# Kernel optimization log

Measured on AMD Instinct MI355X. Metric: run time of the kernel, lower is better.

Reference implementation:

```python
import jax, jax.numpy as jnp
import numpy as np

D = 1024
H = 16
DH = D // H  # 64

def setup_inputs() -> dict:
    key = jax.random.key(0)
    ks = jax.random.split(key, 9)
    B, S = 2, 2048
    s = 1.0 / np.sqrt(D)
    return {
        "embed": jax.random.normal(ks[0], (B, S, D), dtype=jnp.float32),
        "Wq": jax.random.normal(ks[1], (D, D), dtype=jnp.float32) * s,
        "Wk": jax.random.normal(ks[2], (D, D), dtype=jnp.float32) * s,
        "Wv": jax.random.normal(ks[3], (D, D), dtype=jnp.float32) * s,
        "bv": jax.random.normal(ks[4], (D,), dtype=jnp.float32) * 0.01,
        "W1": jax.random.normal(ks[5], (2 * D, D), dtype=jnp.float32) * s,
        "b1": jax.random.normal(ks[6], (2 * D,), dtype=jnp.float32) * 0.01,
        "W2": jax.random.normal(ks[7], (D, 2 * D), dtype=jnp.float32) * (1.0 / np.sqrt(2 * D)),
        "b2": jax.random.normal(ks[8], (D,), dtype=jnp.float32) * 0.01,
    }

def reference(embed, Wq, Wk, Wv, bv, W1, b1, W2, b2):
    B, S, _ = embed.shape
    # torch nn.Linear: y = x @ W.T (+ b)
    Q = embed @ Wq.T                      # [B,S,D]
    K = embed @ Wk.T                      # [B,S,D]
    V = embed @ Wv.T + bv                 # [B,S,D]
    # split heads: the per-head python loop in the original is a vmap over H
    Qh = Q.reshape(B, S, H, DH)
    Kh = K.reshape(B, S, H, DH)
    Vh = V.reshape(B, S, H, DH)
    scores = jnp.einsum('bqhd,bkhd->bhqk', Qh, Kh) / np.sqrt(DH)
    attn = jax.nn.softmax(scores, axis=-1)          # [B,H,S,S]
    out = jnp.einsum('bhqk,bkhd->bqhd', attn, Vh).reshape(B, S, D)
    # FFN (use_ffn)
    out = jax.nn.relu(out @ W1.T + b1) @ W2.T + b2
    # residual (use_residue)
    return out + embed
```

## Files before the change

### kernel.cpp

```cpp
#include <hip/hip_runtime.h>
#include <hip/hip_bf16.h>

typedef unsigned short u16;
typedef unsigned int u32;
typedef __attribute__((ext_vector_type(8))) short short8;
typedef __attribute__((ext_vector_type(4))) short short4v;
typedef __attribute__((ext_vector_type(4))) float f32x4;
typedef __attribute__((ext_vector_type(4))) u16 u16x4;
typedef __attribute__((ext_vector_type(4))) u32 u32x4;

__device__ __forceinline__ u16 f2bf(float f) {
  unsigned u = __builtin_bit_cast(unsigned, f);
  u = (u + 0x7FFFu + ((u >> 16) & 1u)) >> 16;
  return (u16)u;
}

__device__ __forceinline__ u32 cvt_pk_bf16(float lo, float hi) {
  u32 r;
  asm("v_cvt_pk_bf16_f32 %0, %1, %2" : "=v"(r) : "v"(lo), "v"(hi));
  return r;
}

__device__ __forceinline__ void gload16(const void* g, void* l) {
  __builtin_amdgcn_global_load_lds(
      (const __attribute__((address_space(1))) void*)g,
      (__attribute__((address_space(3))) void*)l, 16, 0, 0);
}

__global__ __launch_bounds__(256) void cvt_all(
    const float* __restrict__ e, const float* __restrict__ wq,
    const float* __restrict__ wk, const float* __restrict__ wv,
    const float* __restrict__ w1, const float* __restrict__ w2,
    u16* __restrict__ ebf, u16* __restrict__ wqkv,
    u16* __restrict__ w1b, u16* __restrict__ w2b)
{
  int i = blockIdx.x * 256 + threadIdx.x;
  const float* src;
  u16* dst;
  if (i < 1048576)       { src = e;  dst = ebf; }
  else if (i < 1310720)  { src = wq; dst = wqkv;           i -= 1048576; }
  else if (i < 1572864)  { src = wk; dst = wqkv + 1048576; i -= 1310720; }
  else if (i < 1835008)  { src = wv; dst = wqkv + 2097152; i -= 1572864; }
  else if (i < 2359296)  { src = w1; dst = w1b;            i -= 1835008; }
  else                   { src = w2; dst = w2b;            i -= 2359296; }
  const float4 v = reinterpret_cast<const float4*>(src)[i];
  u16x4 o = { f2bf(v.x), f2bf(v.y), f2bf(v.z), f2bf(v.w) };
  *reinterpret_cast<u16x4*>(dst + (size_t)i * 4) = o;
}

template<int MODE, int BM>
__global__ __launch_bounds__(256, 3) void gemm_bt(
    const u16* __restrict__ A, const u16* __restrict__ W,
    const float* __restrict__ bias, const float* __restrict__ resid,
    void* __restrict__ out0, void* __restrict__ out1, void* __restrict__ out2,
    int M, int N, int K)
{
  constexpr int II = BM / 32;
  __shared__ __align__(16) u16 At[BM * 64];
  __shared__ __align__(16) u16 Bt[128 * 64];
  const int tid = threadIdx.x, lane = tid & 63, wid = tid >> 6;
  const int g = lane >> 4, c = lane & 15;
  const int wr = (wid >> 1) * (BM / 2), wc = (wid & 1) * 64;
  const int m0 = blockIdx.y * BM, n0 = blockIdx.x * 128;
  const int lrow = lane >> 3;
  const int lch = (lane & 7) ^ lrow;
  const int rsw = c & 7;

  f32x4 acc[II][4];
  #pragma unroll
  for (int i = 0; i < II; i++)
    #pragma unroll
    for (int j = 0; j < 4; j++)
      acc[i][j] = (f32x4){0.f, 0.f, 0.f, 0.f};

  const u16* Ab = A + (size_t)m0 * K;
  const u16* Wb = W + (size_t)n0 * K;

  for (int k0 = 0; k0 < K; k0 += 64) {
    __syncthreads();
    #pragma unroll
    for (int i = 0; i < II; i++) {
      const int r0 = (wid * II + i) * 8;
      gload16(Ab + (size_t)(r0 + lrow) * K + k0 + lch * 8, &At[r0 * 64]);
    }
    #pragma unroll
    for (int i = 0; i < 4; i++) {
      const int r0 = (wid * 4 + i) * 8;
      gload16(Wb + (size_t)(r0 + lrow) * K + k0 + lch * 8, &Bt[r0 * 64]);
    }
    __syncthreads();
    #pragma unroll
    for (int kh = 0; kh < 2; kh++) {
      short8 af[II], bw[4];
      #pragma unroll
      for (int i = 0; i < II; i++)
        af[i] = *reinterpret_cast<const short8*>(
            &At[(wr + i * 16 + c) * 64 + (((g + 4 * kh) ^ rsw) * 8)]);
      #pragma unroll
      for (int j = 0; j < 4; j++)
        bw[j] = *reinterpret_cast<const short8*>(
            &Bt[(wc + j * 16 + c) * 64 + (((g + 4 * kh) ^ rsw) * 8)]);
      #pragma unroll
      for (int i = 0; i < II; i++)
        #pragma unroll
        for (int j = 0; j < 4; j++)
          acc[i][j] = __builtin_amdgcn_mfma_f32_16x16x32_bf16(af[i], bw[j], acc[i][j], 0, 0, 0);
    }
  }

  #pragma unroll
  for (int i = 0; i < II; i++) {
    #pragma unroll
    for (int j = 0; j < 4; j++) {
      const int n = n0 + wc + j * 16 + c;
      const int mb = m0 + wr + i * 16 + g * 4;
      if (MODE == 1) {
        const int seg = n >> 10, nn = n & 1023;
        const int h = nn >> 6, d = nn & 63;
        const int bb = mb >> 11, s = mb & 2047;
        if (seg == 2) {
          const float bval = bias[nn];
          u16x4 o;
          #pragma unroll
          for (int r = 0; r < 4; r++) o[r] = f2bf(acc[i][j][r] + bval);
          *reinterpret_cast<u16x4*>(reinterpret_cast<u16*>(out2) +
              ((size_t)((bb << 4) + h) * 64 + d) * 2048 + s) = o;
        } else {
          u16* dst = reinterpret_cast<u16*>(seg ? out1 : out0);
          const float sc = seg ? 1.0f : 0.18033688f;
          #pragma unroll
          for (int r = 0; r < 4; r++)
            dst[((size_t)((bb << 4) + h) * 2048 + s + r) * 64 + d] = f2bf(acc[i][j][r] * sc);
        }
      } else if (MODE == 3) {
        const float bval = bias[n];
        #pragma unroll
        for (int r = 0; r < 4; r++) {
          float v = fmaxf(acc[i][j][r] + bval, 0.f);
          reinterpret_cast<u16*>(out0)[(size_t)(mb + r) * N + n] = f2bf(v);
        }
      } else {
        const float bval = bias[n];
        #pragma unroll
        for (int r = 0; r < 4; r++) {
          const int m = mb + r;
          reinterpret_cast<float*>(out0)[(size_t)m * N + n] =
              acc[i][j][r] + bval + resid[(size_t)m * N + n];
        }
      }
    }
  }
}

__global__ __launch_bounds__(256, 4) void attn_kernel(
    const u16* __restrict__ Qh, const u16* __restrict__ Kh,
    const u16* __restrict__ Vt, u16* __restrict__ ao)
{
  __shared__ __align__(16) u16 Kt[2][64 * 64];
  __shared__ __align__(16) u16 Vl[2][64 * 64];

  const int tid = threadIdx.x;
  const int lane = tid & 63, wid = tid >> 6;
  const int g = lane >> 4, c = lane & 15;
  const int bh = blockIdx.y;
  const int q0 = blockIdx.x * 64 + wid * 16;
  const int lrow = lane >> 3;
  const int lch = (lane & 7) ^ lrow;
  const int rsw = c & 7;

  const u16* qrow = Qh + ((size_t)bh * 2048 + q0 + c) * 64;
  const short8 bqa = *reinterpret_cast<const short8*>(qrow + g * 8);
  const short8 bqb = *reinterpret_cast<const short8*>(qrow + 32 + g * 8);

  f32x4 acc[4];
  #pragma unroll
  for (int dt = 0; dt < 4; dt++) acc[dt] = (f32x4){0.f, 0.f, 0.f, 0.f};
  float l_run = 0.f;

  const u16* Kb = Kh + (size_t)bh * 2048 * 64;
  const u16* Vb = Vt + (size_t)bh * 64 * 2048;

  auto stage = [&](int buf, int t0) {
    #pragma unroll
    for (int i = 0; i < 2; i++) {
      const int r0 = (wid * 2 + i) * 8;
      gload16(Kb + (size_t)(t0 + r0 + lrow) * 64 + lch * 8, &Kt[buf][r0 * 64]);
    }
    #pragma unroll
    for (int i = 0; i < 2; i++) {
      const int r0 = (wid * 2 + i) * 8;
      gload16(Vb + (size_t)(r0 + lrow) * 2048 + t0 + lch * 8, &Vl[buf][r0 * 64]);
    }
  };

  stage(0, 0);

  int cur = 0;
  for (int t0 = 0; t0 < 2048; t0 += 64, cur ^= 1) {
    __syncthreads();
    if (t0 + 64 < 2048) stage(cur ^ 1, t0 + 64);

    #pragma unroll
    for (int cp = 0; cp < 2; cp++) {
      f32x4 sv[2];
      __builtin_amdgcn_s_setprio(1);
      #pragma unroll
      for (int h = 0; h < 2; h++) {
        const u16* kr = &Kt[cur][(cp * 32 + h * 16 + c) * 64];
        short8 ka  = *reinterpret_cast<const short8*>(kr + ((g ^ rsw) * 8));
        short8 ka2 = *reinterpret_cast<const short8*>(kr + (((g + 4) ^ rsw) * 8));
        f32x4 z = (f32x4){0.f, 0.f, 0.f, 0.f};
        z = __builtin_amdgcn_mfma_f32_16x16x32_bf16(ka, bqa, z, 0, 0, 0);
        z = __builtin_amdgcn_mfma_f32_16x16x32_bf16(ka2, bqb, z, 0, 0, 0);
        sv[h] = z;
      }
      __builtin_amdgcn_s_setprio(0);

      float p[8];
      #pragma unroll
      for (int i = 0; i < 8; i++)
        p[i] = __builtin_amdgcn_exp2f(sv[i >> 2][i & 3]);
      l_run += ((p[0] + p[1]) + (p[2] + p[3])) + ((p[4] + p[5]) + (p[6] + p[7]));
      u32x4 w;
      #pragma unroll
      for (int k = 0; k < 4; k++)
        w[k] = cvt_pk_bf16(p[2 * k], p[2 * k + 1]);
      const short8 pk = __builtin_bit_cast(short8, w);

      __builtin_amdgcn_s_setprio(1);
      #pragma unroll
      for (int dt = 0; dt < 4; dt++) {
        const u16* vr = &Vl[cur][(dt * 16 + c) * 64];
        const int ch0 = cp * 4 + (g >> 1);
        const int sub = (g & 1) * 4;
        short4v va  = *reinterpret_cast<const short4v*>(vr + ((ch0 ^ rsw) * 8) + sub);
        short4v vb2 = *reinterpret_cast<const short4v*>(vr + (((ch0 + 2) ^ rsw) * 8) + sub);
        short8 vf = __builtin_shufflevector(va, vb2, 0, 1, 2, 3, 4, 5, 6, 7);
        acc[dt] = __builtin_amdgcn_mfma_f32_16x16x32_bf16(pk, vf, acc[dt], 0, 0, 0);
      }
      __builtin_amdgcn_s_setprio(0);
    }
  }

  float l = l_run;
  l += __shfl_xor(l, 16);
  l += __shfl_xor(l, 32);
  float lq[4];
  #pragma unroll
  for (int r = 0; r < 4; r++) lq[r] = 1.0f / __shfl(l, g * 4 + r);
  u16* ob = ao + (size_t)(bh >> 4) * 2048 * 1024 + (bh & 15) * 64;
  #pragma unroll
  for (int dt = 0; dt < 4; dt++)
    #pragma unroll
    for (int r = 0; r < 4; r++) {
      const size_t q = q0 + g * 4 + r;
      ob[q * 1024 + dt * 16 + c] = f2bf(acc[dt][r] * lq[r]);
    }
}

extern "C" void kernel_launch(void* const* d_in, const int* in_sizes, int n_in,
                              void* d_out, int out_size, void* d_ws, size_t ws_size,
                              hipStream_t stream) {
  const float* embed = (const float*)d_in[0];
  const float* Wq = (const float*)d_in[1];
  const float* Wk = (const float*)d_in[2];
  const float* Wv = (const float*)d_in[3];
  const float* bv = (const float*)d_in[4];
  const float* W1 = (const float*)d_in[5];
  const float* b1 = (const float*)d_in[6];
  const float* W2 = (const float*)d_in[7];
  const float* b2 = (const float*)d_in[8];

  char* ws = (char*)d_ws;
  u16* ebf  = (u16*)ws;  ws += (size_t)4096 * 1024 * 2;
  u16* wqkv = (u16*)ws;  ws += (size_t)3072 * 1024 * 2;
  u16* w1b  = (u16*)ws;  ws += (size_t)2048 * 1024 * 2;
  u16* w2b  = (u16*)ws;  ws += (size_t)1024 * 2048 * 2;
  u16* Qh   = (u16*)ws;  ws += (size_t)4096 * 1024 * 2;
  u16* Kh   = (u16*)ws;  ws += (size_t)4096 * 1024 * 2;
  u16* Vt   = (u16*)ws;  ws += (size_t)4096 * 1024 * 2;
  u16* ao   = (u16*)ws;  ws += (size_t)4096 * 1024 * 2;
  u16* h1   = (u16*)ws;  ws += (size_t)4096 * 2048 * 2;

  dim3 blk(256);
  cvt_all<<<dim3(11264), blk, 0, stream>>>(embed, Wq, Wk, Wv, W1, W2,
                                           ebf, wqkv, w1b, w2b);
  gemm_bt<1, 128><<<dim3(24, 32), blk, 0, stream>>>(
      ebf, wqkv, bv, nullptr, Qh, Kh, Vt, 4096, 3072, 1024);
  attn_kernel<<<dim3(32, 32), blk, 0, stream>>>(Qh, Kh, Vt, ao);
  gemm_bt<3, 128><<<dim3(16, 32), blk, 0, stream>>>(
      ao, w1b, b1, nullptr, h1, nullptr, nullptr, 4096, 2048, 1024);
  gemm_bt<4, 64><<<dim3(8, 64), blk, 0, stream>>>(
      h1, w2b, b2, embed, d_out, nullptr, nullptr, 4096, 1024, 2048);
}
```

Baseline: 154.5 us.

## Process two query tiles per wave in attention and permute V layout

Measured after the change: 144.3 us. 1.07x faster.

```diff
diff --git a/kernel.cpp b/kernel.cpp
--- a/kernel.cpp
+++ b/kernel.cpp
@@ -4,7 +4,6 @@
 typedef unsigned short u16;
 typedef unsigned int u32;
 typedef __attribute__((ext_vector_type(8))) short short8;
-typedef __attribute__((ext_vector_type(4))) short short4v;
 typedef __attribute__((ext_vector_type(4))) float f32x4;
 typedef __attribute__((ext_vector_type(4))) u16 u16x4;
 typedef __attribute__((ext_vector_type(4))) u32 u32x4;
@@ -123,8 +122,10 @@
           u16x4 o;
           #pragma unroll
           for (int r = 0; r < 4; r++) o[r] = f2bf(acc[i][j][r] + bval);
+          const int s32 = s & 31;
+          const int t2 = (s & ~31) + ((s32 >> 2) & 3) * 8 + ((s32 >> 4) & 1) * 4;
           *reinterpret_cast<u16x4*>(reinterpret_cast<u16*>(out2) +
-              ((size_t)((bb << 4) + h) * 64 + d) * 2048 + s) = o;
+              ((size_t)((bb << 4) + h) * 64 + d) * 2048 + t2) = o;
         } else {
           u16* dst = reinterpret_cast<u16*>(seg ? out1 : out0);
           const float sc = seg ? 1.0f : 0.18033688f;
@@ -152,7 +153,7 @@
   }
 }
 
-__global__ __launch_bounds__(256, 4) void attn_kernel(
+__global__ __launch_bounds__(256, 2) void attn_kernel(
     const u16* __restrict__ Qh, const u16* __restrict__ Kh,
     const u16* __restrict__ Vt, u16* __restrict__ ao)
 {
@@ -163,19 +164,27 @@
   const int lane = tid & 63, wid = tid >> 6;
   const int g = lane >> 4, c = lane & 15;
   const int bh = blockIdx.y;
-  const int q0 = blockIdx.x * 64 + wid * 16;
+  const int q0 = blockIdx.x * 128 + wid * 32;
   const int lrow = lane >> 3;
   const int lch = (lane & 7) ^ lrow;
   const int rsw = c & 7;
 
-  const u16* qrow = Qh + ((size_t)bh * 2048 + q0 + c) * 64;
-  const short8 bqa = *reinterpret_cast<const short8*>(qrow + g * 8);
-  const short8 bqb = *reinterpret_cast<const short8*>(qrow + 32 + g * 8);
-
-  f32x4 acc[4];
-  #pragma unroll
-  for (int dt = 0; dt < 4; dt++) acc[dt] = (f32x4){0.f, 0.f, 0.f, 0.f};
-  float l_run = 0.f;
+  short8 bq[2][2];
+  #pragma unroll
+  for (int qt = 0; qt < 2; qt++) {
+    const u16* qrow = Qh + ((size_t)bh * 2048 + q0 + qt * 16 + c) * 64;
+    bq[qt][0] = *reinterpret_cast<const short8*>(qrow + g * 8);
+    bq[qt][1] = *reinterpret_cast<const short8*>(qrow + 32 + g * 8);
+  }
+
+  f32x4 acc[2][4];
+  #pragma unroll
+  for (int qt = 0; qt < 2; qt++)
+    #pragma unroll
+    for (int dt = 0; dt < 4; dt++)
+      acc[qt][dt] = (f32x4){0.f, 0.f, 0.f, 0.f};
+  f32x4 accl[2] = {(f32x4){0.f, 0.f, 0.f, 0.f}, (f32x4){0.f, 0.f, 0.f, 0.f}};
+  const short8 ones = {0x3F80, 0x3F80, 0x3F80, 0x3F80, 0x3F80, 0x3F80, 0x3F80, 0x3F80};
 
   const u16* Kb = Kh + (size_t)bh * 2048 * 64;
   const u16* Vb = Vt + (size_t)bh * 64 * 2048;
@@ -202,60 +211,65 @@
 
     #pragma unroll
     for (int cp = 0; cp < 2; cp++) {
-      f32x4 sv[2];
+      f32x4 sv[2][2];
       __builtin_amdgcn_s_setprio(1);
       #pragma unroll
       for (int h = 0; h < 2; h++) {
         const u16* kr = &Kt[cur][(cp * 32 + h * 16 + c) * 64];
         short8 ka  = *reinterpret_cast<const short8*>(kr + ((g ^ rsw) * 8));
         short8 ka2 = *reinterpret_cast<const short8*>(kr + (((g + 4) ^ rsw) * 8));
-        f32x4 z = (f32x4){0.f, 0.f, 0.f, 0.f};
-        z = __builtin_amdgcn_mfma_f32_16x16x32_bf16(ka, bqa, z, 0, 0, 0);
-        z = __builtin_amdgcn_mfma_f32_16x16x32_bf16(ka2, bqb, z, 0, 0, 0);
-        sv[h] = z;
+        #pragma unroll
+        for (int qt = 0; qt < 2; qt++) {
+          f32x4 z = (f32x4){0.f, 0.f, 0.f, 0.f};
+          z = __builtin_amdgcn_mfma_f32_16x16x32_bf16(ka, bq[qt][0], z, 0, 0, 0);
+          z = __builtin_amdgcn_mfma_f32_16x16x32_bf16(ka2, bq[qt][1], z, 0, 0, 0);
+          sv[qt][h] = z;
+        }
       }
       __builtin_amdgcn_s_setprio(0);
 
-      float p[8];
-      #pragma unroll
-      for (int i = 0; i < 8; i++)
-        p[i] = __builtin_amdgcn_exp2f(sv[i >> 2][i & 3]);
-      l_run += ((p[0] + p[1]) + (p[2] + p[3])) + ((p[4] + p[5]) + (p[6] + p[7]));
-      u32x4 w;
-      #pragma unroll
-      for (int k = 0; k < 4; k++)
-        w[k] = cvt_pk_bf16(p[2 * k], p[2 * k + 1]);
-      const short8 pk = __builtin_bit_cast(short8, w);
+      short8 pk[2];
+      #pragma unroll
+      for (int qt = 0; qt < 2; qt++) {
+        float p[8];
+        #pragma unroll
+        for (int i = 0; i < 8; i++)
+          p[i] = __builtin_amdgcn_exp2f(sv[qt][i >> 2][i & 3]);
+        u32x4 w;
+        #pragma unroll
+        for (int k = 0; k < 4; k++)
+          w[k] = cvt_pk_bf16(p[2 * k], p[2 * k + 1]);
+        pk[qt] = __builtin_bit_cast(short8, w);
+      }
 
       __builtin_amdgcn_s_setprio(1);
       #pragma unroll
       for (int dt = 0; dt < 4; dt++) {
-        const u16* vr = &Vl[cur][(dt * 16 + c) * 64];
-        const int ch0 = cp * 4 + (g >> 1);
-        const int sub = (g & 1) * 4;
-        short4v va  = *reinterpret_cast<const short4v*>(vr + ((ch0 ^ rsw) * 8) + sub);
-        short4v vb2 = *reinterpret_cast<const short4v*>(vr + (((ch0 + 2) ^ rsw) * 8) + sub);
-        short8 vf = __builtin_shufflevector(va, vb2, 0, 1, 2, 3, 4, 5, 6, 7);
-        acc[dt] = __builtin_amdgcn_mfma_f32_16x16x32_bf16(pk, vf, acc[dt], 0, 0, 0);
-      }
+        const short8 vf = *reinterpret_cast<const short8*>(
+            &Vl[cur][(dt * 16 + c) * 64 + (((cp * 4 + g) ^ rsw) * 8)]);
+        acc[0][dt] = __builtin_amdgcn_mfma_f32_16x16x32_bf16(pk[0], vf, acc[0][dt], 0, 0, 0);
+        acc[1][dt] = __builtin_amdgcn_mfma_f32_16x16x32_bf16(pk[1], vf, acc[1][dt], 0, 0, 0);
+      }
+      accl[0] = __builtin_amdgcn_mfma_f32_16x16x32_bf16(pk[0], ones, accl[0], 0, 0, 0);
+      accl[1] = __builtin_amdgcn_mfma_f32_16x16x32_bf16(pk[1], ones, accl[1], 0, 0, 0);
       __builtin_amdgcn_s_setprio(0);
     }
   }
 
-  float l = l_run;
-  l += __shfl_xor(l, 16);
-  l += __shfl_xor(l, 32);
-  float lq[4];
-  #pragma unroll
-  for (int r = 0; r < 4; r++) lq[r] = 1.0f / __shfl(l, g * 4 + r);
   u16* ob = ao + (size_t)(bh >> 4) * 2048 * 1024 + (bh & 15) * 64;
   #pragma unroll
-  for (int dt = 0; dt < 4; dt++)
-    #pragma unroll
-    for (int r = 0; r < 4; r++) {
-      const size_t q = q0 + g * 4 + r;
-      ob[q * 1024 + dt * 16 + c] = f2bf(acc[dt][r] * lq[r]);
-    }
+  for (int qt = 0; qt < 2; qt++) {
+    float lq[4];
+    #pragma unroll
+    for (int r = 0; r < 4; r++) lq[r] = 1.0f / accl[qt][r];
+    #pragma unroll
+    for (int dt = 0; dt < 4; dt++)
+      #pragma unroll
+      for (int r = 0; r < 4; r++) {
+        const size_t q = q0 + qt * 16 + g * 4 + r;
+        ob[q * 1024 + dt * 16 + c] = f2bf(acc[qt][dt][r] * lq[r]);
+      }
+  }
 }
 
 extern "C" void kernel_launch(void* const* d_in, const int* in_sizes, int n_in,
@@ -287,7 +301,7 @@
                                            ebf, wqkv, w1b, w2b);
   gemm_bt<1, 128><<<dim3(24, 32), blk, 0, stream>>>(
       ebf, wqkv, bv, nullptr, Qh, Kh, Vt, 4096, 3072, 1024);
-  attn_kernel<<<dim3(32, 32), blk, 0, stream>>>(Qh, Kh, Vt, ao);
+  attn_kernel<<<dim3(16, 32), blk, 0, stream>>>(Qh, Kh, Vt, ao);
   gemm_bt<3, 128><<<dim3(16, 32), blk, 0, stream>>>(
       ao, w1b, b1, nullptr, h1, nullptr, nullptr, 4096, 2048, 1024);
   gemm_bt<4, 64><<<dim3(8, 64), blk, 0, stream>>>(
```
